# Kernel tuning notes

Measured on AMD Instinct MI355X. Metric: run time of the kernel, lower is better.

## Reference

```python
import jax, jax.numpy as jnp
import numpy as np

D_MODEL = 2048
N_HEADS = 16
N_KV_HEADS = 4
HEAD_DIM = 128
ROPE_THETA = 1000000.0
B, T = 2, 2048


def setup_inputs() -> dict:
    key = jax.random.key(0)
    ks = jax.random.split(key, 5)
    s_in = 1.0 / np.sqrt(D_MODEL)
    s_o = 1.0 / np.sqrt(N_HEADS * HEAD_DIM)
    return {
        "x": jax.random.normal(ks[0], (B, T, D_MODEL), jnp.float32),
        "w_q": jax.random.normal(ks[1], (N_HEADS * HEAD_DIM, D_MODEL), jnp.float32) * s_in,
        "w_k": jax.random.normal(ks[2], (N_KV_HEADS * HEAD_DIM, D_MODEL), jnp.float32) * s_in,
        "w_v": jax.random.normal(ks[3], (N_KV_HEADS * HEAD_DIM, D_MODEL), jnp.float32) * s_in,
        "w_o": jax.random.normal(ks[4], (D_MODEL, N_HEADS * HEAD_DIM), jnp.float32) * s_o,
    }


def _rope_cos_sin(T, dtype):
    # inv_freq over even dims, emb = concat(freqs, freqs) (HF/llama convention)
    inv_freq = 1.0 / (ROPE_THETA ** (jnp.arange(0, HEAD_DIM, 2, dtype=jnp.float32) / HEAD_DIM))
    freqs = jnp.arange(T, dtype=jnp.float32)[:, None] * inv_freq[None, :]  # [T, hd/2]
    emb = jnp.concatenate([freqs, freqs], axis=-1)  # [T, hd]
    return jnp.cos(emb).astype(dtype), jnp.sin(emb).astype(dtype)


def _rotate_half(x):
    x1, x2 = jnp.split(x, 2, axis=-1)
    return jnp.concatenate([-x2, x1], axis=-1)


def reference(x, w_q, w_k, w_v, w_o):
    B, T, D = x.shape
    # QKV projections (bias=False), split heads -> [B, H, T, hd]
    q = (x @ w_q.T).reshape(B, T, N_HEADS, HEAD_DIM).transpose(0, 2, 1, 3)
    k = (x @ w_k.T).reshape(B, T, N_KV_HEADS, HEAD_DIM).transpose(0, 2, 1, 3)
    v = (x @ w_v.T).reshape(B, T, N_KV_HEADS, HEAD_DIM).transpose(0, 2, 1, 3)
    # RoPE
    cos, sin = _rope_cos_sin(T, x.dtype)  # [T, hd]
    q = q * cos + _rotate_half(q) * sin
    k = k * cos + _rotate_half(k) * sin
    # GQA: expand kv heads (repeat_interleave over head dim)
    rep = N_HEADS // N_KV_HEADS
    k = jnp.repeat(k, rep, axis=1)
    v = jnp.repeat(v, rep, axis=1)
    # Eager attention: QK^T * scale + causal mask, softmax, PV
    scale = HEAD_DIM ** -0.5
    scores = jnp.einsum("bhtd,bhsd->bhts", q, k) * scale
    causal = jnp.tril(jnp.ones((T, T), dtype=bool))
    scores = jnp.where(causal[None, None], scores, jnp.finfo(scores.dtype).min)
    probs = jax.nn.softmax(scores, axis=-1)
    out = jnp.einsum("bhts,bhsd->bhtd", probs, v)  # [B, H, T, hd]
    out = out.transpose(0, 2, 1, 3).reshape(B, T, N_HEADS * HEAD_DIM)
    return out @ w_o.T
```

## Files before the change

kernel.cpp:

```cpp
#include <hip/hip_runtime.h>
#include <cstdint>
#include <cstddef>

typedef unsigned short u16;
typedef unsigned u32;
typedef unsigned long long u64;
typedef __attribute__((ext_vector_type(8))) short short8;
typedef __attribute__((ext_vector_type(4))) float f32x4;

#define T_SEQ 2048
#define DM    2048
#define NHEAD 16
#define NKV   4
#define HD    128
#define NEGBIG (-3.0e38f)
#define QSCALE 0.1275525165017459f
#define L2IF (-0.31143258583318043f)

__device__ __forceinline__ u16 f2bf(float f) {
  union { float f; unsigned u; } c; c.f = f;
  return (u16)((c.u + 0x7fffu + ((c.u >> 16) & 1u)) >> 16);
}
__device__ __forceinline__ float bf2f(u16 b) {
  union { float f; unsigned u; } c; c.u = ((unsigned)b) << 16;
  return c.f;
}
__device__ __forceinline__ void gl_lds16(const u16* g, u16* l) {
  __builtin_amdgcn_global_load_lds(
      (const __attribute__((address_space(1))) void*)g,
      (__attribute__((address_space(3))) void*)l, 16, 0, 0);
}

__global__ void castk_all(const float* __restrict__ x, const float* __restrict__ wq,
                          const float* __restrict__ wk, const float* __restrict__ wv,
                          const float* __restrict__ wo, u16* __restrict__ dst) {
  long long i4 = (long long)blockIdx.x * 256 + threadIdx.x;
  const float* src; long long off;
  if (i4 < (2LL << 20))                    { src = x;  off = i4; }
  else if (i4 < (3LL << 20))               { src = wq; off = i4 - (2LL << 20); }
  else if (i4 < (3LL << 20) + (1 << 18))   { src = wk; off = i4 - (3LL << 20); }
  else if (i4 < (3LL << 20) + (2 << 18))   { src = wv; off = i4 - (3LL << 20) - (1 << 18); }
  else                                     { src = wo; off = i4 - (3LL << 20) - (2 << 18); }
  float4 v = *(const float4*)(src + off * 4);
  u16* d = dst + i4 * 4;
  d[0] = f2bf(v.x); d[1] = f2bf(v.y); d[2] = f2bf(v.z); d[3] = f2bf(v.w);
}

__global__ void ropek(u16* __restrict__ buf) {
  int idx = blockIdx.x * 256 + threadIdx.x;
  int r = idx >> 6, i = idx & 63;
  int t = r & (T_SEQ - 1);
  float inv = exp2f((float)i * L2IF);
  float ang = (float)t * inv;
  float c = cosf(ang), s = sinf(ang);
  size_t base = (size_t)r * HD + i;
  float x1 = bf2f(buf[base]), x2 = bf2f(buf[base + 64]);
  buf[base]      = f2bf(x1 * c - x2 * s);
  buf[base + 64] = f2bf(x2 * c + x1 * s);
}

template <int MODE>
__global__ __launch_bounds__(256) void gemm_bt(
    const u16* __restrict__ A, const u16* __restrict__ Bm,
    void* __restrict__ Out0, u16* __restrict__ OutK, u16* __restrict__ OutV,
    int M, int N, int K) {
  __shared__ __align__(16) u16 As[2][128 * 32];
  __shared__ __align__(16) u16 Bs[2][128 * 32];
  const int tid = threadIdx.x;
  const int w = tid >> 6, l = tid & 63;
  const int lm = l & 15, q = l >> 4;
  const int m0 = blockIdx.y * 128, n0 = blockIdx.x * 128;
  const int mq = w & 1, nq = w >> 1;
  const u16* Ab = A + (size_t)m0 * K;
  const u16* Bb = Bm + (size_t)n0 * K;

  const int s0_ = w * 64 + l, s1_ = 256 + s0_;
  const int row0 = s0_ >> 2, kq0 = (s0_ & 3) * 8;
  const int row1 = s1_ >> 2, kq1 = (s1_ & 3) * 8;

  f32x4 acc[4][4] = {};
  const int nk = K >> 5;

  gl_lds16(Ab + (size_t)row0 * K + kq0, &As[0][s0_ * 8]);
  gl_lds16(Bb + (size_t)row0 * K + kq0, &Bs[0][s0_ * 8]);
  gl_lds16(Ab + (size_t)row1 * K + kq1, &As[0][s1_ * 8]);
  gl_lds16(Bb + (size_t)row1 * K + kq1, &Bs[0][s1_ * 8]);
  __syncthreads();

  for (int ki = 0; ki < nk; ++ki) {
    const int bb = ki & 1;
    if (ki + 1 < nk) {
      const int k0 = (ki + 1) << 5;
      gl_lds16(Ab + (size_t)row0 * K + k0 + kq0, &As[bb ^ 1][s0_ * 8]);
      gl_lds16(Bb + (size_t)row0 * K + k0 + kq0, &Bs[bb ^ 1][s0_ * 8]);
      gl_lds16(Ab + (size_t)row1 * K + k0 + kq1, &As[bb ^ 1][s1_ * 8]);
      gl_lds16(Bb + (size_t)row1 * K + k0 + kq1, &Bs[bb ^ 1][s1_ * 8]);
    }
    short8 af[4], bf[4];
#pragma unroll
    for (int i = 0; i < 4; ++i) {
      af[i] = *(const short8*)(&As[bb][(mq * 64 + i * 16 + lm) * 32 + q * 8]);
      bf[i] = *(const short8*)(&Bs[bb][(nq * 64 + i * 16 + lm) * 32 + q * 8]);
    }
#pragma unroll
    for (int i = 0; i < 4; ++i)
#pragma unroll
      for (int j = 0; j < 4; ++j)
        acc[i][j] = __builtin_amdgcn_mfma_f32_16x16x32_bf16(af[i], bf[j], acc[i][j], 0, 0, 0);
    __syncthreads();
  }

#pragma unroll
  for (int i = 0; i < 4; ++i)
#pragma unroll
    for (int j = 0; j < 4; ++j)
#pragma unroll
      for (int r = 0; r < 4; ++r) {
        int m = m0 + mq * 64 + i * 16 + q * 4 + r;
        int n = n0 + nq * 64 + j * 16 + lm;
        float v = acc[i][j][r];
        if constexpr (MODE == 0) {
          ((float*)Out0)[(size_t)m * N + n] = v;
        } else {
          int b = m >> 11, t = m & (T_SEQ - 1);
          if (n < 2048) {
            int h = n >> 7, d = n & (HD - 1);
            ((u16*)Out0)[(((size_t)(b * NHEAD + h)) * T_SEQ + t) * HD + d] = f2bf(v * QSCALE);
          } else if (n < 2560) {
            int nn = n - 2048, h = nn >> 7, d = nn & (HD - 1);
            OutK[(((size_t)(b * NKV + h)) * T_SEQ + t) * HD + d] = f2bf(v);
          } else {
            int nn = n - 2560, h = nn >> 7, d = nn & (HD - 1);
            OutV[(((size_t)(b * NKV + h)) * HD + d) * T_SEQ + t] = f2bf(v);
          }
        }
      }
}

#define PSTRIDE 72
__global__ __launch_bounds__(256, 2) void attnk(
    const u16* __restrict__ Q, const u16* __restrict__ Kh,
    const u16* __restrict__ Vt, u16* __restrict__ Oa) {
  __shared__ __align__(16) u16 Ks[2][64 * 128];
  __shared__ __align__(16) u16 Vs[2][128 * 64];
  __shared__ __align__(16) u16 Pl[4][16 * PSTRIDE];
  const int tid = threadIdx.x;
  const int w = tid >> 6, l = tid & 63, lm = l & 15, q = l >> 4;
  const int bh = blockIdx.y, b = bh >> 4, h = bh & 15, kvh = h >> 2;
  const u16* Kb = Kh + ((size_t)(b * NKV + kvh)) * T_SEQ * HD;
  const u16* Vb = Vt + ((size_t)(b * NKV + kvh)) * HD * T_SEQ;
  u16* Pw = Pl[w];
  const int p = blockIdx.x;

  const int r16 = tid >> 4, c16 = tid & 15;
  const int r8  = tid >> 3, c8  = tid & 7;

#pragma unroll 1
  for (int half = 0; half < 2; ++half) {
    const int tile = half ? p : (31 - p);
    const int tbase = tile * 64 + w * 16;
    const u16* Qb = Q + (((size_t)(b * NHEAD + h)) * T_SEQ + tbase) * HD;

    short8 qa[4];
#pragma unroll
    for (int ks = 0; ks < 4; ++ks)
      qa[ks] = *(const short8*)(Qb + (size_t)lm * HD + ks * 32 + q * 8);

    {
      const float tf = (float)(tbase + lm);
#pragma unroll
      for (int ks = 0; ks < 2; ++ks) {
        short8 lo = qa[ks], hi = qa[ks + 2];
#pragma unroll
        for (int e = 0; e < 8; ++e) {
          int d = ks * 32 + q * 8 + e;
          float ang = tf * exp2f((float)d * L2IF);
          float sn, cs;
          sincosf(ang, &sn, &cs);
          float x1 = bf2f((u16)lo[e]), x2 = bf2f((u16)hi[e]);
          lo[e] = (short)f2bf(x1 * cs - x2 * sn);
          hi[e] = (short)f2bf(x2 * cs + x1 * sn);
        }
        qa[ks] = lo; qa[ks + 2] = hi;
      }
    }

    float m_i = NEGBIG, l_i = 0.f;
    f32x4 oacc[8] = {};
    const int nst = tile + 1;

    {
#pragma unroll
      for (int j = 0; j < 4; ++j) {
        int s = j * 16 + r16, g = c16 ^ (s & 15);
        gl_lds16(Kb + (size_t)s * HD + g * 8, &Ks[0][s * 128 + c16 * 8]);
      }
#pragma unroll
      for (int j = 0; j < 4; ++j) {
        int d = j * 32 + r8, g = c8 ^ (d & 7);
        gl_lds16(Vb + (size_t)d * T_SEQ + g * 8, &Vs[0][d * 64 + c8 * 8]);
      }
    }
    __syncthreads();

    for (int st = 0; st < nst; ++st) {
      const int bb = st & 1;
      if (st + 1 < nst) {
        const int s0n = (st + 1) * 64;
#pragma unroll
        for (int j = 0; j < 4; ++j) {
          int s = j * 16 + r16, g = c16 ^ (s & 15);
          gl_lds16(Kb + (size_t)(s0n + s) * HD + g * 8, &Ks[bb ^ 1][s * 128 + c16 * 8]);
        }
#pragma unroll
        for (int j = 0; j < 4; ++j) {
          int d = j * 32 + r8, g = c8 ^ (d & 7);
          gl_lds16(Vb + (size_t)d * T_SEQ + s0n + g * 8, &Vs[bb ^ 1][d * 64 + c8 * 8]);
        }
      }

      f32x4 sacc[4] = {};
#pragma unroll
      for (int ks = 0; ks < 4; ++ks)
#pragma unroll
        for (int nt = 0; nt < 4; ++nt) {
          short8 kb = *(const short8*)(&Ks[bb][(nt * 16 + lm) * 128 + ((ks * 4 + q) ^ lm) * 8]);
          sacc[nt] = __builtin_amdgcn_mfma_f32_16x16x32_bf16(kb, qa[ks], sacc[nt], 0, 0, 0);
        }

      const bool diag = (st == nst - 1);
      const int s0 = st * 64;
      float mx = m_i;
      float pe[4][4];
#pragma unroll
      for (int nt = 0; nt < 4; ++nt)
#pragma unroll
        for (int j = 0; j < 4; ++j) {
          float v = sacc[nt][j];
          if (diag) {
            int s_abs = s0 + nt * 16 + q * 4 + j;
            if (s_abs > tbase + lm) v = NEGBIG;
          }
          pe[nt][j] = v;
          mx = fmaxf(mx, v);
        }
      mx = fmaxf(mx, __shfl_xor(mx, 16, 64));
      mx = fmaxf(mx, __shfl_xor(mx, 32, 64));
      float alpha = exp2f(m_i - mx);
      float sum = 0.f;
#pragma unroll
      for (int nt = 0; nt < 4; ++nt) {
        float e0 = exp2f(pe[nt][0] - mx), e1 = exp2f(pe[nt][1] - mx);
        float e2 = exp2f(pe[nt][2] - mx), e3 = exp2f(pe[nt][3] - mx);
        sum += (e0 + e1) + (e2 + e3);
        u32 lo32 = __builtin_amdgcn_perm(__float_as_uint(e1), __float_as_uint(e0), 0x07060302u);
        u32 hi32 = __builtin_amdgcn_perm(__float_as_uint(e3), __float_as_uint(e2), 0x07060302u);
        *(u64*)(Pw + lm * PSTRIDE + nt * 16 + q * 4) = ((u64)hi32 << 32) | lo32;
      }
      sum += __shfl_xor(sum, 16, 64);
      sum += __shfl_xor(sum, 32, 64);
      bool bump = (mx > m_i);
      m_i = mx;
      l_i = l_i * alpha + sum;

      if (__any(bump)) {
#pragma unroll
        for (int dt = 0; dt < 8; ++dt)
#pragma unroll
          for (int j = 0; j < 4; ++j) oacc[dt][j] *= alpha;
      }

      asm volatile("" ::: "memory");

#pragma unroll
      for (int ks = 0; ks < 2; ++ks) {
        short8 pa = *(const short8*)(Pw + lm * PSTRIDE + ks * 32 + q * 8);
#pragma unroll
        for (int dt = 0; dt < 8; ++dt) {
          short8 vb = *(const short8*)(
              &Vs[bb][(dt * 16 + lm) * 64 + ((ks * 4 + q) ^ (lm & 7)) * 8]);
          oacc[dt] = __builtin_amdgcn_mfma_f32_16x16x32_bf16(vb, pa, oacc[dt], 0, 0, 0);
        }
      }
      __syncthreads();
    }

    float inv = 1.0f / l_i;
    int t = tbase + lm;
#pragma unroll
    for (int dt = 0; dt < 8; ++dt) {
      u16 ok[4];
#pragma unroll
      for (int j = 0; j < 4; ++j) ok[j] = f2bf(oacc[dt][j] * inv);
      *(u64*)(Oa + ((size_t)(b * T_SEQ + t)) * (NHEAD * HD) + h * HD + dt * 16 + q * 4) =
          (u64)ok[0] | ((u64)ok[1] << 16) | ((u64)ok[2] << 32) | ((u64)ok[3] << 48);
    }
  }
}

extern "C" void kernel_launch(void* const* d_in, const int* in_sizes, int n_in,
                              void* d_out, int out_size, void* d_ws, size_t ws_size,
                              hipStream_t stream) {
  const float* x  = (const float*)d_in[0];
  const float* wq = (const float*)d_in[1];
  const float* wk = (const float*)d_in[2];
  const float* wv = (const float*)d_in[3];
  const float* wo = (const float*)d_in[4];
  float* out = (float*)d_out;

  u16* ws  = (u16*)d_ws;
  u16* xb  = ws;
  u16* wqb = xb  + (8u << 20);
  u16* wkb = wqb + (4u << 20);
  u16* wvb = wkb + (1u << 20);
  u16* wob = wvb + (1u << 20);
  u16* Qb  = wob + (4u << 20);
  u16* Kb  = Qb  + (8u << 20);
  u16* Vtb = Kb  + (2u << 20);
  u16* Ab  = xb;

  castk_all<<<18432, 256, 0, stream>>>(x, wq, wk, wv, wo, ws);

  gemm_bt<3><<<dim3(24, 32), 256, 0, stream>>>(xb, wqb, Qb, Kb, Vtb, 4096, 3072, 2048);

  ropek<<<4096, 256, 0, stream>>>(Kb);

  attnk<<<dim3(16, 32), 256, 0, stream>>>(Qb, Kb, Vtb, Ab);

  gemm_bt<0><<<dim3(16, 32), 256, 0, stream>>>(Ab, wob, out, nullptr, nullptr, 4096, 2048, 2048);
}
```

Baseline: 299.2 us.

## Enlarge attention query tile to 128 rows, two 16-row subtiles per wave

Each wave of the attention kernel now handles 32 query rows instead of 16, so every K/V tile staged in LDS feeds twice as many MFMAs. This halves the grid, keeps the causal load balancing by pairing tiles p and 15-p, and skips key tiles lying entirely beyond the wave's causal range. The cost is roughly double the accumulator registers, hence launch bounds drop to one block per SIMD group, which lowers occupancy. With only 256 blocks on a large GPU, this also risks underfilling the compute units.

```diff
diff --git a/kernel.cpp b/kernel.cpp
--- a/kernel.cpp
+++ b/kernel.cpp
@@ -138,12 +138,12 @@
 }
 
 #define PSTRIDE 72
-__global__ __launch_bounds__(256, 2) void attnk(
+__global__ __launch_bounds__(256, 1) void attnk(
     const u16* __restrict__ Q, const u16* __restrict__ Kh,
     const u16* __restrict__ Vt, u16* __restrict__ Oa) {
   __shared__ __align__(16) u16 Ks[2][64 * 128];
   __shared__ __align__(16) u16 Vs[2][128 * 64];
-  __shared__ __align__(16) u16 Pl[4][16 * PSTRIDE];
+  __shared__ __align__(16) u16 Pl[4][32 * PSTRIDE];
   const int tid = threadIdx.x;
   const int w = tid >> 6, l = tid & 63, lm = l & 15, q = l >> 4;
   const int bh = blockIdx.y, b = bh >> 4, h = bh & 15, kvh = h >> 2;
@@ -157,20 +157,23 @@
 
 #pragma unroll 1
   for (int half = 0; half < 2; ++half) {
-    const int tile = half ? p : (31 - p);
-    const int tbase = tile * 64 + w * 16;
-    const u16* Qb = Q + (((size_t)(b * NHEAD + h)) * T_SEQ + tbase) * HD;
-
-    short8 qa[4];
-#pragma unroll
-    for (int ks = 0; ks < 4; ++ks)
-      qa[ks] = *(const short8*)(Qb + (size_t)lm * HD + ks * 32 + q * 8);
-
-    {
-      const float tf = (float)(tbase + lm);
+    const int tile = half ? p : (15 - p);
+    const int twave = tile * 128 + w * 32;
+    const u16* Qb = Q + (((size_t)(b * NHEAD + h)) * T_SEQ + twave) * HD;
+
+    short8 qa[2][4];
+#pragma unroll
+    for (int nt2 = 0; nt2 < 2; ++nt2)
+#pragma unroll
+      for (int ks = 0; ks < 4; ++ks)
+        qa[nt2][ks] = *(const short8*)(Qb + (size_t)(nt2 * 16 + lm) * HD + ks * 32 + q * 8);
+
+#pragma unroll
+    for (int nt2 = 0; nt2 < 2; ++nt2) {
+      const float tf = (float)(twave + nt2 * 16 + lm);
 #pragma unroll
       for (int ks = 0; ks < 2; ++ks) {
-        short8 lo = qa[ks], hi = qa[ks + 2];
+        short8 lo = qa[nt2][ks], hi = qa[nt2][ks + 2];
 #pragma unroll
         for (int e = 0; e < 8; ++e) {
           int d = ks * 32 + q * 8 + e;
@@ -181,25 +184,23 @@
           lo[e] = (short)f2bf(x1 * cs - x2 * sn);
           hi[e] = (short)f2bf(x2 * cs + x1 * sn);
         }
-        qa[ks] = lo; qa[ks + 2] = hi;
-      }
-    }
-
-    float m_i = NEGBIG, l_i = 0.f;
-    f32x4 oacc[8] = {};
-    const int nst = tile + 1;
-
-    {
-#pragma unroll
-      for (int j = 0; j < 4; ++j) {
-        int s = j * 16 + r16, g = c16 ^ (s & 15);
-        gl_lds16(Kb + (size_t)s * HD + g * 8, &Ks[0][s * 128 + c16 * 8]);
-      }
-#pragma unroll
-      for (int j = 0; j < 4; ++j) {
-        int d = j * 32 + r8, g = c8 ^ (d & 7);
-        gl_lds16(Vb + (size_t)d * T_SEQ + g * 8, &Vs[0][d * 64 + c8 * 8]);
-      }
+        qa[nt2][ks] = lo; qa[nt2][ks + 2] = hi;
+      }
+    }
+
+    float m_i[2] = {NEGBIG, NEGBIG}, l_i[2] = {0.f, 0.f};
+    f32x4 oacc[2][8] = {};
+    const int nst = 2 * (tile + 1);
+
+#pragma unroll
+    for (int j = 0; j < 4; ++j) {
+      int s = j * 16 + r16, g = c16 ^ (s & 15);
+      gl_lds16(Kb + (size_t)s * HD + g * 8, &Ks[0][s * 128 + c16 * 8]);
+    }
+#pragma unroll
+    for (int j = 0; j < 4; ++j) {
+      int d = j * 32 + r8, g = c8 ^ (d & 7);
+      gl_lds16(Vb + (size_t)d * T_SEQ + g * 8, &Vs[0][d * 64 + c8 * 8]);
     }
     __syncthreads();
 
@@ -219,81 +220,97 @@
         }
       }
 
-      f32x4 sacc[4] = {};
-#pragma unroll
-      for (int ks = 0; ks < 4; ++ks)
-#pragma unroll
-        for (int nt = 0; nt < 4; ++nt) {
-          short8 kb = *(const short8*)(&Ks[bb][(nt * 16 + lm) * 128 + ((ks * 4 + q) ^ lm) * 8]);
-          sacc[nt] = __builtin_amdgcn_mfma_f32_16x16x32_bf16(kb, qa[ks], sacc[nt], 0, 0, 0);
-        }
-
-      const bool diag = (st == nst - 1);
       const int s0 = st * 64;
-      float mx = m_i;
-      float pe[4][4];
-#pragma unroll
-      for (int nt = 0; nt < 4; ++nt)
-#pragma unroll
-        for (int j = 0; j < 4; ++j) {
-          float v = sacc[nt][j];
-          if (diag) {
-            int s_abs = s0 + nt * 16 + q * 4 + j;
-            if (s_abs > tbase + lm) v = NEGBIG;
+      if (s0 <= twave + 31) {
+        f32x4 sacc[4][2] = {};
+#pragma unroll
+        for (int ks = 0; ks < 4; ++ks)
+#pragma unroll
+          for (int nt = 0; nt < 4; ++nt) {
+            short8 kb = *(const short8*)(&Ks[bb][(nt * 16 + lm) * 128 + ((ks * 4 + q) ^ lm) * 8]);
+            sacc[nt][0] = __builtin_amdgcn_mfma_f32_16x16x32_bf16(kb, qa[0][ks], sacc[nt][0], 0, 0, 0);
+            sacc[nt][1] = __builtin_amdgcn_mfma_f32_16x16x32_bf16(kb, qa[1][ks], sacc[nt][1], 0, 0, 0);
           }
-          pe[nt][j] = v;
-          mx = fmaxf(mx, v);
-        }
-      mx = fmaxf(mx, __shfl_xor(mx, 16, 64));
-      mx = fmaxf(mx, __shfl_xor(mx, 32, 64));
-      float alpha = exp2f(m_i - mx);
-      float sum = 0.f;
-#pragma unroll
-      for (int nt = 0; nt < 4; ++nt) {
-        float e0 = exp2f(pe[nt][0] - mx), e1 = exp2f(pe[nt][1] - mx);
-        float e2 = exp2f(pe[nt][2] - mx), e3 = exp2f(pe[nt][3] - mx);
-        sum += (e0 + e1) + (e2 + e3);
-        u32 lo32 = __builtin_amdgcn_perm(__float_as_uint(e1), __float_as_uint(e0), 0x07060302u);
-        u32 hi32 = __builtin_amdgcn_perm(__float_as_uint(e3), __float_as_uint(e2), 0x07060302u);
-        *(u64*)(Pw + lm * PSTRIDE + nt * 16 + q * 4) = ((u64)hi32 << 32) | lo32;
-      }
-      sum += __shfl_xor(sum, 16, 64);
-      sum += __shfl_xor(sum, 32, 64);
-      bool bump = (mx > m_i);
-      m_i = mx;
-      l_i = l_i * alpha + sum;
-
-      if (__any(bump)) {
-#pragma unroll
-        for (int dt = 0; dt < 8; ++dt)
-#pragma unroll
-          for (int j = 0; j < 4; ++j) oacc[dt][j] *= alpha;
-      }
-
-      asm volatile("" ::: "memory");
-
-#pragma unroll
-      for (int ks = 0; ks < 2; ++ks) {
-        short8 pa = *(const short8*)(Pw + lm * PSTRIDE + ks * 32 + q * 8);
-#pragma unroll
-        for (int dt = 0; dt < 8; ++dt) {
-          short8 vb = *(const short8*)(
-              &Vs[bb][(dt * 16 + lm) * 64 + ((ks * 4 + q) ^ (lm & 7)) * 8]);
-          oacc[dt] = __builtin_amdgcn_mfma_f32_16x16x32_bf16(vb, pa, oacc[dt], 0, 0, 0);
+
+        const bool diag = (s0 + 64 > twave);
+        float al[2];
+        bool bump = false;
+#pragma unroll
+        for (int nt2 = 0; nt2 < 2; ++nt2) {
+          const int t_abs = twave + nt2 * 16 + lm;
+          float mx = m_i[nt2];
+          float pe[4][4];
+#pragma unroll
+          for (int nt = 0; nt < 4; ++nt)
+#pragma unroll
+            for (int j = 0; j < 4; ++j) {
+              float v = sacc[nt][nt2][j];
+              if (diag) {
+                int s_abs = s0 + nt * 16 + q * 4 + j;
+                if (s_abs > t_abs) v = NEGBIG;
+              }
+              pe[nt][j] = v;
+              mx = fmaxf(mx, v);
+            }
+          mx = fmaxf(mx, __shfl_xor(mx, 16, 64));
+          mx = fmaxf(mx, __shfl_xor(mx, 32, 64));
+          al[nt2] = exp2f(m_i[nt2] - mx);
+          float sum = 0.f;
+#pragma unroll
+          for (int nt = 0; nt < 4; ++nt) {
+            float e0 = exp2f(pe[nt][0] - mx), e1 = exp2f(pe[nt][1] - mx);
+            float e2 = exp2f(pe[nt][2] - mx), e3 = exp2f(pe[nt][3] - mx);
+            sum += (e0 + e1) + (e2 + e3);
+            u32 lo32 = __builtin_amdgcn_perm(__float_as_uint(e1), __float_as_uint(e0), 0x07060302u);
+            u32 hi32 = __builtin_amdgcn_perm(__float_as_uint(e3), __float_as_uint(e2), 0x07060302u);
+            *(u64*)(Pw + (nt2 * 16 + lm) * PSTRIDE + nt * 16 + q * 4) = ((u64)hi32 << 32) | lo32;
+          }
+          sum += __shfl_xor(sum, 16, 64);
+          sum += __shfl_xor(sum, 32, 64);
+          bump = bump || (mx > m_i[nt2]);
+          m_i[nt2] = mx;
+          l_i[nt2] = l_i[nt2] * al[nt2] + sum;
+        }
+
+        if (__any(bump)) {
+#pragma unroll
+          for (int nt2 = 0; nt2 < 2; ++nt2)
+#pragma unroll
+            for (int dt = 0; dt < 8; ++dt)
+#pragma unroll
+              for (int j = 0; j < 4; ++j) oacc[nt2][dt][j] *= al[nt2];
+        }
+
+        asm volatile("" ::: "memory");
+
+#pragma unroll
+        for (int ks = 0; ks < 2; ++ks) {
+          short8 pa0 = *(const short8*)(Pw + lm * PSTRIDE + ks * 32 + q * 8);
+          short8 pa1 = *(const short8*)(Pw + (16 + lm) * PSTRIDE + ks * 32 + q * 8);
+#pragma unroll
+          for (int dt = 0; dt < 8; ++dt) {
+            short8 vb = *(const short8*)(
+                &Vs[bb][(dt * 16 + lm) * 64 + ((ks * 4 + q) ^ (lm & 7)) * 8]);
+            oacc[0][dt] = __builtin_amdgcn_mfma_f32_16x16x32_bf16(vb, pa0, oacc[0][dt], 0, 0, 0);
+            oacc[1][dt] = __builtin_amdgcn_mfma_f32_16x16x32_bf16(vb, pa1, oacc[1][dt], 0, 0, 0);
+          }
         }
       }
       __syncthreads();
     }
 
-    float inv = 1.0f / l_i;
-    int t = tbase + lm;
-#pragma unroll
-    for (int dt = 0; dt < 8; ++dt) {
-      u16 ok[4];
-#pragma unroll
-      for (int j = 0; j < 4; ++j) ok[j] = f2bf(oacc[dt][j] * inv);
-      *(u64*)(Oa + ((size_t)(b * T_SEQ + t)) * (NHEAD * HD) + h * HD + dt * 16 + q * 4) =
-          (u64)ok[0] | ((u64)ok[1] << 16) | ((u64)ok[2] << 32) | ((u64)ok[3] << 48);
+#pragma unroll
+    for (int nt2 = 0; nt2 < 2; ++nt2) {
+      float inv = 1.0f / l_i[nt2];
+      int t = twave + nt2 * 16 + lm;
+#pragma unroll
+      for (int dt = 0; dt < 8; ++dt) {
+        u16 ok[4];
+#pragma unroll
+        for (int j = 0; j < 4; ++j) ok[j] = f2bf(oacc[nt2][dt][j] * inv);
+        *(u64*)(Oa + ((size_t)(b * T_SEQ + t)) * (NHEAD * HD) + h * HD + dt * 16 + q * 4) =
+            (u64)ok[0] | ((u64)ok[1] << 16) | ((u64)ok[2] << 32) | ((u64)ok[3] << 48);
+      }
     }
   }
 }
@@ -325,7 +342,7 @@
 
   ropek<<<4096, 256, 0, stream>>>(Kb);
 
-  attnk<<<dim3(16, 32), 256, 0, stream>>>(Qb, Kb, Vtb, Ab);
+  attnk<<<dim3(8, 32), 256, 0, stream>>>(Qb, Kb, Vtb, Ab);
 
   gemm_bt<0><<<dim3(16, 32), 256, 0, stream>>>(Ab, wob, out, nullptr, nullptr, 4096, 2048, 2048);
 }
```

After: 335.7 us. +12.2%, slower.
